# Performance work log

Measured on AMD Instinct MI355X. Metric: run time of the kernel, lower is better.

## Reference

```python
import jax, jax.numpy as jnp
import numpy as np

B, N, C, NH = 4, 2304, 256, 8
HD = C // NH            # head dim = 32
HS = WS = 48            # H = W = sqrt(N)
RADIUS = 3.0
MLP_HID = 4 * C
SCALE = HD ** (-0.5)
NEG = -1e9              # stands in for -inf (identical softmax up to fp eps)
EPS = 1e-6


def spatial_mask():
    # get_spatial_mask: cdist of (y, x) grid coords, -inf where dist > radius
    yy, xx = jnp.meshgrid(jnp.arange(HS), jnp.arange(WS), indexing='ij')
    coords = jnp.stack([yy, xx], -1).reshape(-1, 2).astype(jnp.float32)  # [N, 2]
    d2 = jnp.sum((coords[:, None, :] - coords[None, :, :]) ** 2, -1)     # [N, N]
    return jnp.where(d2 > RADIUS * RADIUS, NEG, 0.0)


def layernorm(x, g, b):
    mu = jnp.mean(x, -1, keepdims=True)
    var = jnp.mean((x - mu) ** 2, -1, keepdims=True)
    return (x - mu) * jax.lax.rsqrt(var + EPS) * g + b


def setup_inputs() -> dict:
    key = jax.random.key(0)
    ks = jax.random.split(key, 16)
    s = 0.02
    return {
        'x':    jax.random.normal(ks[0], (B, N, C), jnp.float32),
        'x_kv': jax.random.normal(ks[1], (B, N, C), jnp.float32),
        'Wq': jax.random.normal(ks[2], (C, C), jnp.float32) * s,
        'bq': jnp.zeros((C,), jnp.float32),
        'Wk': jax.random.normal(ks[3], (C, C), jnp.float32) * s,
        'bk': jnp.zeros((C,), jnp.float32),
        'Wv': jax.random.normal(ks[4], (C, C), jnp.float32) * s,
        'bv': jnp.zeros((C,), jnp.float32),
        'Wp': jax.random.normal(ks[5], (C, C), jnp.float32) * s,
        'bp': jnp.zeros((C,), jnp.float32),
        'g1': jnp.ones((C,), jnp.float32),
        'b1': jnp.zeros((C,), jnp.float32),
        'g2': jnp.ones((C,), jnp.float32),
        'b2': jnp.zeros((C,), jnp.float32),
        'W1': jax.random.normal(ks[6], (C, MLP_HID), jnp.float32) * s,
        'bm1': jnp.zeros((MLP_HID,), jnp.float32),
        'W2': jax.random.normal(ks[7], (MLP_HID, C), jnp.float32) * s,
        'bm2': jnp.zeros((C,), jnp.float32),
    }


def reference(x, x_kv, Wq, bq, Wk, bk, Wv, bv, Wp, bp,
              g1, b1, g2, b2, W1, bm1, W2, bm2):
    mask = spatial_mask()                                  # [N, N]
    h = layernorm(x, g1, b1)
    hkv = layernorm(x_kv, g1, b1)
    q = (h @ Wq + bq).reshape(B, N, NH, HD)
    k = (hkv @ Wk + bk).reshape(B, N, NH, HD)
    v = (hkv @ Wv + bv).reshape(B, N, NH, HD)
    scores = jnp.einsum('bqhd,bkhd->bhqk', q, k) * SCALE + mask
    attn = jax.nn.softmax(scores, axis=-1)
    out = jnp.einsum('bhqk,bkhd->bqhd', attn, v).reshape(B, N, C)
    x = x + out @ Wp + bp
    m = layernorm(x, g2, b2)
    x = x + jax.nn.gelu(m @ W1 + bm1, approximate=False) @ W2 + bm2
    return x
```

## Files before the change

### kernel.cpp

```cpp
#include <hip/hip_runtime.h>
#include <hip/hip_fp16.h>
#include <math.h>

#define BB 4
#define NN 2304
#define CC 256
#define HS 48
#define HID 1024
#define BNROWS (BB * NN)
#define ATTN_SCALE 0.17677669529663687f

typedef _Float16 f16;
typedef __attribute__((ext_vector_type(2))) _Float16 h2;
typedef __attribute__((ext_vector_type(8))) _Float16 h8;
typedef __attribute__((ext_vector_type(4))) float f4;

#define GLLS16(g, l)                                                        \
    __builtin_amdgcn_global_load_lds(                                       \
        (const __attribute__((address_space(1))) unsigned int*)(g),         \
        (__attribute__((address_space(3))) unsigned int*)(l), 16, 0, 0)
#define WAIT_VM0()   asm volatile("s_waitcnt vmcnt(0)" ::: "memory")
#define WAIT_VM6()   asm volatile("s_waitcnt vmcnt(6)" ::: "memory")
#define WAIT_LGKM0() asm volatile("s_waitcnt lgkmcnt(0)" ::: "memory")

static __device__ __forceinline__ float wave_sum64(float v) {
    v += __shfl_xor(v, 32, 64);
    v += __shfl_xor(v, 16, 64);
    v += __shfl_xor(v, 8, 64);
    v += __shfl_xor(v, 4, 64);
    v += __shfl_xor(v, 2, 64);
    v += __shfl_xor(v, 1, 64);
    return v;
}

__global__ __launch_bounds__(256) void prep_ln1_kernel(
    const float* __restrict__ x, const float* __restrict__ xkv,
    const float* __restrict__ Wq, const float* __restrict__ Wk,
    const float* __restrict__ Wv, const float* __restrict__ Wp,
    const float* __restrict__ W1, const float* __restrict__ W2,
    const float* __restrict__ bq, const float* __restrict__ bk,
    const float* __restrict__ bv,
    const float* __restrict__ g, const float* __restrict__ be,
    f16* __restrict__ WqkvT, f16* __restrict__ WpT,
    f16* __restrict__ W1T, f16* __restrict__ W2T, float* __restrict__ bqkv,
    f16* __restrict__ hq, f16* __restrict__ hkv)
{
    __shared__ float tt[32][33];
    int bx = blockIdx.x;
    const int tid = threadIdx.x;
    if (bx < 768) {
        const float* src; f16* dst; int K, N;
        if (bx < 64)        { src = Wq; dst = WqkvT;           K = 256;  N = 256; }
        else if (bx < 128)  { src = Wk; dst = WqkvT + 65536;   K = 256;  N = 256;  bx -= 64; }
        else if (bx < 192)  { src = Wv; dst = WqkvT + 131072;  K = 256;  N = 256;  bx -= 128; }
        else if (bx < 256)  { src = Wp; dst = WpT;             K = 256;  N = 256;  bx -= 192; }
        else if (bx < 512)  { src = W1; dst = W1T;             K = 256;  N = 1024; bx -= 256; }
        else                { src = W2; dst = W2T;             K = 1024; N = 256;  bx -= 512; }
        const int tN = N >> 5;
        const int kt = bx / tN, nt = bx - kt * tN;
        const int rr = tid >> 5, cc = tid & 31;
#pragma unroll
        for (int j = 0; j < 4; ++j)
            tt[rr + 8 * j][cc] = src[(size_t)(kt * 32 + rr + 8 * j) * N + nt * 32 + cc];
        __syncthreads();
#pragma unroll
        for (int j = 0; j < 4; ++j)
            dst[(size_t)(nt * 32 + rr + 8 * j) * K + kt * 32 + cc] = (f16)tt[cc][rr + 8 * j];
        return;
    }
    if (bx == 768) {
        if (tid < 256) {
            bqkv[tid]       = bq[tid];
            bqkv[tid + 256] = bk[tid];
            bqkv[tid + 512] = bv[tid];
        }
        return;
    }
    const int r = (bx - 769) * 4 + (tid >> 6);
    const int lane = tid & 63;
    const float* src; f16* dst;
    if (r < BNROWS) { src = x + (size_t)r * CC;              dst = hq + (size_t)r * CC; }
    else { src = xkv + (size_t)(r - BNROWS) * CC; dst = hkv + (size_t)(r - BNROWS) * CC; }
    const float4 v = ((const float4*)src)[lane];
    const float mu = wave_sum64(v.x + v.y + v.z + v.w) * (1.0f / CC);
    const float d0 = v.x - mu, d1 = v.y - mu, d2 = v.z - mu, d3 = v.w - mu;
    const float var = wave_sum64(d0 * d0 + d1 * d1 + d2 * d2 + d3 * d3) * (1.0f / CC);
    const float rs = rsqrtf(var + 1e-6f);
    const float4 g4 = ((const float4*)g)[lane];
    const float4 b4 = ((const float4*)be)[lane];
    h2 o01 = (h2){(f16)(d0 * rs * g4.x + b4.x), (f16)(d1 * rs * g4.y + b4.y)};
    h2 o23 = (h2){(f16)(d2 * rs * g4.z + b4.z), (f16)(d3 * rs * g4.w + b4.w)};
    ((h2*)dst)[lane * 2] = o01;
    ((h2*)dst)[lane * 2 + 1] = o23;
}

__global__ __launch_bounds__(256) void ln2_kernel(
    const f16* __restrict__ x1, const float* __restrict__ g,
    const float* __restrict__ be, f16* __restrict__ m2)
{
    const int r = blockIdx.x * 4 + (threadIdx.x >> 6);
    const int lane = threadIdx.x & 63;
    const f16* src = x1 + (size_t)r * CC;
    const h2 a01 = ((const h2*)src)[lane * 2];
    const h2 a23 = ((const h2*)src)[lane * 2 + 1];
    const float v0 = (float)a01[0], v1 = (float)a01[1];
    const float v2 = (float)a23[0], v3 = (float)a23[1];
    const float mu = wave_sum64(v0 + v1 + v2 + v3) * (1.0f / CC);
    const float d0 = v0 - mu, d1 = v1 - mu, d2 = v2 - mu, d3 = v3 - mu;
    const float var = wave_sum64(d0 * d0 + d1 * d1 + d2 * d2 + d3 * d3) * (1.0f / CC);
    const float rs = rsqrtf(var + 1e-6f);
    const float4 g4 = ((const float4*)g)[lane];
    const float4 b4 = ((const float4*)be)[lane];
    f16* dst = m2 + (size_t)r * CC;
    h2 o01 = (h2){(f16)(d0 * rs * g4.x + b4.x), (f16)(d1 * rs * g4.y + b4.y)};
    h2 o23 = (h2){(f16)(d2 * rs * g4.z + b4.z), (f16)(d3 * rs * g4.w + b4.w)};
    ((h2*)dst)[lane * 2] = o01;
    ((h2*)dst)[lane * 2 + 1] = o23;
}

template <bool GELU, int RESID, bool OUTF32, bool QKV>
__global__ __launch_bounds__(256, 4) void gemm_wave(
    const f16* __restrict__ Aq, const f16* __restrict__ Akv,
    const f16* __restrict__ Bt, const float* __restrict__ bias,
    const void* __restrict__ resid, void* __restrict__ out1,
    void* __restrict__ outkv, int N, int K)
{
    __shared__ f16 lds[4 * 6144];
    const int tid = threadIdx.x;
    const int wid = tid >> 6, lane = tid & 63;
    const int ln15 = lane & 15, quad = lane >> 4;
    const int jr = lane >> 2, js = lane & 3;
    f16* slot = lds + wid * 6144;
    const int n0 = blockIdx.x * 64;
    const int m0 = (blockIdx.y * 4 + wid) * 32;
    const f16* Ap = QKV ? (n0 < 256 ? Aq : Akv) : Aq;

    size_t ga[2], gb[4];
#pragma unroll
    for (int i = 0; i < 2; ++i) {
        const int r = i * 16 + jr;
        const int q = (js - (r >> 1)) & 3;
        ga[i] = (size_t)(m0 + r) * K + q * 8;
    }
#pragma unroll
    for (int i = 0; i < 4; ++i) {
        const int r = i * 16 + jr;
        const int q = (js - (r >> 1)) & 3;
        gb[i] = (size_t)(n0 + r) * K + q * 8;
    }
    int aoff[2], boff[4];
#pragma unroll
    for (int mt = 0; mt < 2; ++mt) {
        const int r = mt * 16 + ln15;
        aoff[mt] = (r * 4 + ((quad + (r >> 1)) & 3)) * 16;
    }
#pragma unroll
    for (int nt = 0; nt < 4; ++nt) {
        const int r = nt * 16 + ln15;
        boff[nt] = (r * 4 + ((quad + (r >> 1)) & 3)) * 16;
    }

    f4 acc[2][4];
#pragma unroll
    for (int i = 0; i < 2; ++i)
#pragma unroll
        for (int j = 0; j < 4; ++j) acc[i][j] = (f4){0.f, 0.f, 0.f, 0.f};

    {
        f16* Al = slot;
        f16* Bl = slot + 1024;
#pragma unroll
        for (int i = 0; i < 2; ++i) GLLS16(Ap + ga[i], Al + i * 512);
#pragma unroll
        for (int i = 0; i < 4; ++i) GLLS16(Bt + gb[i], Bl + i * 512);
    }

    int cur = 0;
    for (int k0 = 0; k0 < K; k0 += 32) {
        const bool more = (k0 + 32 < K);
        f16* Ac = slot + cur * 3072;
        f16* Bc = Ac + 1024;
        if (more) {
            f16* An = slot + (cur ^ 1) * 3072;
            f16* Bn = An + 1024;
            WAIT_LGKM0();
#pragma unroll
            for (int i = 0; i < 2; ++i) GLLS16(Ap + ga[i] + k0 + 32, An + i * 512);
#pragma unroll
            for (int i = 0; i < 4; ++i) GLLS16(Bt + gb[i] + k0 + 32, Bn + i * 512);
            WAIT_VM6();
        } else {
            WAIT_VM0();
        }
        h8 aF[2], bF[4];
#pragma unroll
        for (int nt = 0; nt < 4; ++nt)
            bF[nt] = *(const h8*)((const char*)Bc + boff[nt]);
#pragma unroll
        for (int mt = 0; mt < 2; ++mt)
            aF[mt] = *(const h8*)((const char*)Ac + aoff[mt]);
#pragma unroll
        for (int mt = 0; mt < 2; ++mt)
#pragma unroll
            for (int nt = 0; nt < 4; ++nt)
                acc[mt][nt] = __builtin_amdgcn_mfma_f32_16x16x32_f16(
                    aF[mt], bF[nt], acc[mt][nt], 0, 0, 0);
        cur ^= 1;
    }

#pragma unroll
    for (int nt = 0; nt < 4; ++nt) {
        const int gn = n0 + nt * 16 + ln15;
        const float bs = bias[gn];
#pragma unroll
        for (int mt = 0; mt < 2; ++mt) {
#pragma unroll
            for (int r = 0; r < 4; ++r) {
                const int gm = m0 + mt * 16 + quad * 4 + r;
                float v = acc[mt][nt][r] + bs;
                if (GELU) v = 0.5f * v * (1.0f + erff(v * 0.70710678118654752f));
                if (RESID == 1) v += ((const float*)resid)[(size_t)gm * N + gn];
                if (RESID == 2) v += (float)((const f16*)resid)[(size_t)gm * N + gn];
                if (QKV) {
                    if (gn < 256) ((f16*)out1)[(size_t)gm * 256 + gn] = (f16)v;
                    else ((f16*)outkv)[(size_t)gm * 512 + (gn - 256)] = (f16)v;
                } else if (OUTF32) {
                    ((float*)out1)[(size_t)gm * N + gn] = v;
                } else {
                    ((f16*)out1)[(size_t)gm * N + gn] = (f16)v;
                }
            }
        }
    }
}

__device__ __constant__ int ATT_DY[29] = {
    -3, -2, -2, -2, -2, -2, -1, -1, -1, -1, -1, 0, 0, 0, 0,
    0, 0, 0, 1, 1, 1, 1, 1, 2, 2, 2, 2, 2, 3};
__device__ __constant__ int ATT_DX[29] = {
    0, -2, -1, 0, 1, 2, -2, -1, 0, 1, 2, -3, -2, -1, 0,
    1, 2, 3, -2, -1, 0, 1, 2, -2, -1, 0, 1, 2, 0};

__global__ __launch_bounds__(128) void attn_tile_kernel(
    const f16* __restrict__ qf, const f16* __restrict__ kvf,
    f16* __restrict__ ao)
{
    __shared__ f16 ks[196][66];
    __shared__ f16 vs[196][66];
    const int tile = blockIdx.x, hp = blockIdx.y, b = blockIdx.z;
    const int ty0 = (tile / 6) * 8, tx0 = (tile - (tile / 6) * 6) * 8;
    const int tid = threadIdx.x;

    for (int idx = tid; idx < 196 * 16; idx += 128) {
        const int r = idx >> 4, seg = idx & 15;
        const int gy = ty0 - 3 + r / 14, gx = tx0 - 3 + (r - (r / 14) * 14);
        uint4 val = {0u, 0u, 0u, 0u};
        if ((unsigned)gy < HS && (unsigned)gx < HS) {
            const size_t rowb = ((size_t)b * NN + gy * HS + gx) * 512;
            const int ch = (seg < 8) ? (hp * 64 + seg * 8)
                                     : (256 + hp * 64 + (seg - 8) * 8);
            val = *(const uint4*)&kvf[rowb + ch];
        }
        f16* dstp = (seg < 8) ? &ks[r][(seg & 7) * 8] : &vs[r][(seg & 7) * 8];
        ((unsigned int*)dstp)[0] = val.x;
        ((unsigned int*)dstp)[1] = val.y;
        ((unsigned int*)dstp)[2] = val.z;
        ((unsigned int*)dstp)[3] = val.w;
    }
    __syncthreads();

    const int q = tid & 63, hh = tid >> 6;
    const int qy = q >> 3, qx = q & 7;
    const size_t qrow = (size_t)b * NN + (ty0 + qy) * HS + tx0 + qx;
    const f16* qp = qf + qrow * CC + hp * 64 + hh * 32;
    uint4 qa[4];
#pragma unroll
    for (int i = 0; i < 4; ++i) qa[i] = ((const uint4*)qp)[i];
    const h2* q2 = (const h2*)qa;

    float s[29];
#pragma unroll
    for (int n = 0; n < 29; ++n) {
        const int dy = ATT_DY[n], dx = ATT_DX[n];
        const int r = (qy + 3 + dy) * 14 + qx + 3 + dx;
        const bool valid = (unsigned)(ty0 + qy + dy) < HS &&
                           (unsigned)(tx0 + qx + dx) < HS;
        float a = 0.0f;
        const h2* kp = (const h2*)&ks[r][hh * 32];
#pragma unroll
        for (int i = 0; i < 16; ++i)
            a = __builtin_amdgcn_fdot2(q2[i], kp[i], a, false);
        s[n] = valid ? a * ATTN_SCALE : -1e30f;
    }
    float m = s[0];
#pragma unroll
    for (int n = 1; n < 29; ++n) m = fmaxf(m, s[n]);
    float l = 0.0f;
#pragma unroll
    for (int n = 0; n < 29; ++n) { s[n] = __expf(s[n] - m); l += s[n]; }
    h2 a2[16];
#pragma unroll
    for (int i = 0; i < 16; ++i) a2[i] = (h2){(f16)0.f, (f16)0.f};
#pragma unroll
    for (int n = 0; n < 29; ++n) {
        const int dy = ATT_DY[n], dx = ATT_DX[n];
        const int r = (qy + 3 + dy) * 14 + qx + 3 + dx;
        const f16 pn = (f16)s[n];
        const h2 ph = (h2){pn, pn};
        const h2* vp = (const h2*)&vs[r][hh * 32];
#pragma unroll
        for (int i = 0; i < 16; ++i) a2[i] += ph * vp[i];
    }
    const float inv = 1.0f / l;
    uint4 ov[4];
    f16* oh = (f16*)ov;
#pragma unroll
    for (int i = 0; i < 16; ++i) {
        oh[2 * i]     = (f16)((float)a2[i][0] * inv);
        oh[2 * i + 1] = (f16)((float)a2[i][1] * inv);
    }
    uint4* dst = (uint4*)(ao + qrow * CC + hp * 64 + hh * 32);
#pragma unroll
    for (int i = 0; i < 4; ++i) dst[i] = ov[i];
}

extern "C" void kernel_launch(void* const* d_in, const int* in_sizes, int n_in,
                              void* d_out, int out_size, void* d_ws, size_t ws_size,
                              hipStream_t stream) {
    const float* x    = (const float*)d_in[0];
    const float* x_kv = (const float*)d_in[1];
    const float* Wq   = (const float*)d_in[2];
    const float* bq   = (const float*)d_in[3];
    const float* Wk   = (const float*)d_in[4];
    const float* bk   = (const float*)d_in[5];
    const float* Wv   = (const float*)d_in[6];
    const float* bv   = (const float*)d_in[7];
    const float* Wp   = (const float*)d_in[8];
    const float* bp   = (const float*)d_in[9];
    const float* g1   = (const float*)d_in[10];
    const float* b1   = (const float*)d_in[11];
    const float* g2   = (const float*)d_in[12];
    const float* b2   = (const float*)d_in[13];
    const float* W1   = (const float*)d_in[14];
    const float* bm1  = (const float*)d_in[15];
    const float* W2   = (const float*)d_in[16];
    const float* bm2  = (const float*)d_in[17];
    float* outp = (float*)d_out;

    f16* wsh = (f16*)d_ws;
    f16* WqkvT = wsh;
    f16* WpT   = wsh + 196608;
    f16* W1T   = wsh + 262144;
    f16* W2T   = wsh + 524288;
    float* bqkv = (float*)(wsh + 786432);
    f16* hq    = wsh + 787968;
    f16* hkv   = wsh + 3147264;
    f16* qf    = wsh + 5506560;
    f16* kvf   = wsh + 7865856;
    f16* ao    = hq;
    f16* x1    = hkv;
    f16* m2    = qf;
    f16* hidF  = kvf;
    const bool fused = ws_size >= (size_t)17303040 * sizeof(f16);

    prep_ln1_kernel<<<5377, 256, 0, stream>>>(
        x, x_kv, Wq, Wk, Wv, Wp, W1, W2, bq, bk, bv, g1, b1,
        WqkvT, WpT, W1T, W2T, bqkv, hq, hkv);
    gemm_wave<false, 0, false, true><<<dim3(12, 72), 256, 0, stream>>>(
        hq, hkv, WqkvT, bqkv, nullptr, qf, kvf, 768, 256);
    attn_tile_kernel<<<dim3(36, 4, BB), 128, 0, stream>>>(qf, kvf, ao);
    gemm_wave<false, 1, false, false><<<dim3(4, 72), 256, 0, stream>>>(
        ao, nullptr, WpT, bp, x, x1, nullptr, 256, 256);
    ln2_kernel<<<BNROWS / 4, 256, 0, stream>>>(x1, g2, b2, m2);
    if (fused) {
        gemm_wave<true, 0, false, false><<<dim3(16, 72), 256, 0, stream>>>(
            m2, nullptr, W1T, bm1, nullptr, hidF, nullptr, 1024, 256);
        gemm_wave<false, 2, true, false><<<dim3(4, 72), 256, 0, stream>>>(
            hidF, nullptr, W2T, bm2, x1, outp, nullptr, 256, 1024);
    } else {
        for (int b = 0; b < BB; ++b) {
            const size_t off = (size_t)b * NN * CC;
            gemm_wave<true, 0, false, false><<<dim3(16, 18), 256, 0, stream>>>(
                m2 + off, nullptr, W1T, bm1, nullptr, hidF, nullptr, 1024, 256);
            gemm_wave<false, 2, true, false><<<dim3(4, 18), 256, 0, stream>>>(
                hidF, nullptr, W2T, bm2, x1 + off, outp + off, nullptr, 256, 1024);
        }
    }
    (void)in_sizes; (void)n_in; (void)out_size;
}
```

Measured before the change: 197.5 us.

## Fuse output projection GEMM with residual add and LayerNorm2 in one kernel

```diff
diff --git a/kernel.cpp b/kernel.cpp
--- a/kernel.cpp
+++ b/kernel.cpp
@@ -94,30 +94,6 @@
     ((h2*)dst)[lane * 2 + 1] = o23;
 }
 
-__global__ __launch_bounds__(256) void ln2_kernel(
-    const f16* __restrict__ x1, const float* __restrict__ g,
-    const float* __restrict__ be, f16* __restrict__ m2)
-{
-    const int r = blockIdx.x * 4 + (threadIdx.x >> 6);
-    const int lane = threadIdx.x & 63;
-    const f16* src = x1 + (size_t)r * CC;
-    const h2 a01 = ((const h2*)src)[lane * 2];
-    const h2 a23 = ((const h2*)src)[lane * 2 + 1];
-    const float v0 = (float)a01[0], v1 = (float)a01[1];
-    const float v2 = (float)a23[0], v3 = (float)a23[1];
-    const float mu = wave_sum64(v0 + v1 + v2 + v3) * (1.0f / CC);
-    const float d0 = v0 - mu, d1 = v1 - mu, d2 = v2 - mu, d3 = v3 - mu;
-    const float var = wave_sum64(d0 * d0 + d1 * d1 + d2 * d2 + d3 * d3) * (1.0f / CC);
-    const float rs = rsqrtf(var + 1e-6f);
-    const float4 g4 = ((const float4*)g)[lane];
-    const float4 b4 = ((const float4*)be)[lane];
-    f16* dst = m2 + (size_t)r * CC;
-    h2 o01 = (h2){(f16)(d0 * rs * g4.x + b4.x), (f16)(d1 * rs * g4.y + b4.y)};
-    h2 o23 = (h2){(f16)(d2 * rs * g4.z + b4.z), (f16)(d3 * rs * g4.w + b4.w)};
-    ((h2*)dst)[lane * 2] = o01;
-    ((h2*)dst)[lane * 2 + 1] = o23;
-}
-
 template <bool GELU, int RESID, bool OUTF32, bool QKV>
 __global__ __launch_bounds__(256, 4) void gemm_wave(
     const f16* __restrict__ Aq, const f16* __restrict__ Akv,
@@ -208,6 +184,11 @@
         cur ^= 1;
     }
 
+    f16* qdst = nullptr; int qstr = 0, qn0 = 0;
+    if (QKV) {
+        if (n0 < 256) { qdst = (f16*)out1;  qstr = 256; qn0 = n0; }
+        else          { qdst = (f16*)outkv; qstr = 512; qn0 = n0 - 256; }
+    }
 #pragma unroll
     for (int nt = 0; nt < 4; ++nt) {
         const int gn = n0 + nt * 16 + ln15;
@@ -222,13 +203,178 @@
                 if (RESID == 1) v += ((const float*)resid)[(size_t)gm * N + gn];
                 if (RESID == 2) v += (float)((const f16*)resid)[(size_t)gm * N + gn];
                 if (QKV) {
-                    if (gn < 256) ((f16*)out1)[(size_t)gm * 256 + gn] = (f16)v;
-                    else ((f16*)outkv)[(size_t)gm * 512 + (gn - 256)] = (f16)v;
+                    qdst[(size_t)gm * qstr + qn0 + nt * 16 + ln15] = (f16)v;
                 } else if (OUTF32) {
                     ((float*)out1)[(size_t)gm * N + gn] = v;
                 } else {
                     ((f16*)out1)[(size_t)gm * N + gn] = (f16)v;
                 }
+            }
+        }
+    }
+}
+
+__global__ __launch_bounds__(256, 3) void gemm_op_ln2(
+    const f16* __restrict__ Aa, const f16* __restrict__ Bt,
+    const float* __restrict__ bias, const float* __restrict__ xres,
+    const float* __restrict__ g, const float* __restrict__ be,
+    f16* __restrict__ x1, f16* __restrict__ m2)
+{
+    __shared__ f16 lds[4 * 6144];
+    __shared__ float sred[32][4][2];
+    const int tid = threadIdx.x;
+    const int wid = tid >> 6, lane = tid & 63;
+    const int ln15 = lane & 15, quad = lane >> 4;
+    const int jr = lane >> 2, js = lane & 3;
+    f16* slot = lds + wid * 6144;
+    const int m0 = blockIdx.x * 32;
+    const int n0 = wid * 64;
+    const int K = 256;
+
+    size_t ga[2], gb[4];
+#pragma unroll
+    for (int i = 0; i < 2; ++i) {
+        const int r = i * 16 + jr;
+        const int q = (js - (r >> 1)) & 3;
+        ga[i] = (size_t)(m0 + r) * K + q * 8;
+    }
+#pragma unroll
+    for (int i = 0; i < 4; ++i) {
+        const int r = i * 16 + jr;
+        const int q = (js - (r >> 1)) & 3;
+        gb[i] = (size_t)(n0 + r) * K + q * 8;
+    }
+    int aoff[2], boff[4];
+#pragma unroll
+    for (int mt = 0; mt < 2; ++mt) {
+        const int r = mt * 16 + ln15;
+        aoff[mt] = (r * 4 + ((quad + (r >> 1)) & 3)) * 16;
+    }
+#pragma unroll
+    for (int nt = 0; nt < 4; ++nt) {
+        const int r = nt * 16 + ln15;
+        boff[nt] = (r * 4 + ((quad + (r >> 1)) & 3)) * 16;
+    }
+
+    f4 acc[2][4];
+#pragma unroll
+    for (int i = 0; i < 2; ++i)
+#pragma unroll
+        for (int j = 0; j < 4; ++j) acc[i][j] = (f4){0.f, 0.f, 0.f, 0.f};
+
+    {
+        f16* Al = slot;
+        f16* Bl = slot + 1024;
+#pragma unroll
+        for (int i = 0; i < 2; ++i) GLLS16(Aa + ga[i], Al + i * 512);
+#pragma unroll
+        for (int i = 0; i < 4; ++i) GLLS16(Bt + gb[i], Bl + i * 512);
+    }
+    int cur = 0;
+    for (int k0 = 0; k0 < K; k0 += 32) {
+        const bool more = (k0 + 32 < K);
+        f16* Ac = slot + cur * 3072;
+        f16* Bc = Ac + 1024;
+        if (more) {
+            f16* An = slot + (cur ^ 1) * 3072;
+            f16* Bn = An + 1024;
+            WAIT_LGKM0();
+#pragma unroll
+            for (int i = 0; i < 2; ++i) GLLS16(Aa + ga[i] + k0 + 32, An + i * 512);
+#pragma unroll
+            for (int i = 0; i < 4; ++i) GLLS16(Bt + gb[i] + k0 + 32, Bn + i * 512);
+            WAIT_VM6();
+        } else {
+            WAIT_VM0();
+        }
+        h8 aF[2], bF[4];
+#pragma unroll
+        for (int nt = 0; nt < 4; ++nt)
+            bF[nt] = *(const h8*)((const char*)Bc + boff[nt]);
+#pragma unroll
+        for (int mt = 0; mt < 2; ++mt)
+            aF[mt] = *(const h8*)((const char*)Ac + aoff[mt]);
+#pragma unroll
+        for (int mt = 0; mt < 2; ++mt)
+#pragma unroll
+            for (int nt = 0; nt < 4; ++nt)
+                acc[mt][nt] = __builtin_amdgcn_mfma_f32_16x16x32_f16(
+                    aF[mt], bF[nt], acc[mt][nt], 0, 0, 0);
+        cur ^= 1;
+    }
+
+    float bsv[4], g2v[4], b2v[4];
+#pragma unroll
+    for (int nt = 0; nt < 4; ++nt) {
+        const int gn = n0 + nt * 16 + ln15;
+        bsv[nt] = bias[gn];
+        g2v[nt] = g[gn];
+        b2v[nt] = be[gn];
+    }
+    float s1[2][4], s2[2][4];
+#pragma unroll
+    for (int mt = 0; mt < 2; ++mt)
+#pragma unroll
+        for (int r = 0; r < 4; ++r) { s1[mt][r] = 0.f; s2[mt][r] = 0.f; }
+#pragma unroll
+    for (int mt = 0; mt < 2; ++mt) {
+#pragma unroll
+        for (int r = 0; r < 4; ++r) {
+            const int gm = m0 + mt * 16 + quad * 4 + r;
+#pragma unroll
+            for (int nt = 0; nt < 4; ++nt) {
+                const int gn = n0 + nt * 16 + ln15;
+                float v = acc[mt][nt][r] + bsv[nt]
+                        + xres[(size_t)gm * CC + gn];
+                acc[mt][nt][r] = v;
+                x1[(size_t)gm * CC + gn] = (f16)v;
+                s1[mt][r] += v;
+                s2[mt][r] += v * v;
+            }
+        }
+    }
+#pragma unroll
+    for (int off = 1; off < 16; off <<= 1) {
+#pragma unroll
+        for (int mt = 0; mt < 2; ++mt)
+#pragma unroll
+            for (int r = 0; r < 4; ++r) {
+                s1[mt][r] += __shfl_xor(s1[mt][r], off, 64);
+                s2[mt][r] += __shfl_xor(s2[mt][r], off, 64);
+            }
+    }
+    if (ln15 == 0) {
+#pragma unroll
+        for (int mt = 0; mt < 2; ++mt)
+#pragma unroll
+            for (int r = 0; r < 4; ++r) {
+                const int rr = mt * 16 + quad * 4 + r;
+                sred[rr][wid][0] = s1[mt][r];
+                sred[rr][wid][1] = s2[mt][r];
+            }
+    }
+    __syncthreads();
+#pragma unroll
+    for (int mt = 0; mt < 2; ++mt) {
+#pragma unroll
+        for (int r = 0; r < 4; ++r) {
+            const int rr = mt * 16 + quad * 4 + r;
+            const int gm = m0 + rr;
+            float a = 0.f, b = 0.f;
+#pragma unroll
+            for (int w = 0; w < 4; ++w) {
+                a += sred[rr][w][0];
+                b += sred[rr][w][1];
+            }
+            const float mu = a * (1.0f / CC);
+            const float var = fmaxf(b * (1.0f / CC) - mu * mu, 0.0f);
+            const float rs = rsqrtf(var + 1e-6f);
+#pragma unroll
+            for (int nt = 0; nt < 4; ++nt) {
+                const int gn = n0 + nt * 16 + ln15;
+                const float v = acc[mt][nt][r];
+                m2[(size_t)gm * CC + gn] =
+                    (f16)((v - mu) * rs * g2v[nt] + b2v[nt]);
             }
         }
     }
@@ -369,9 +515,7 @@
     gemm_wave<false, 0, false, true><<<dim3(12, 72), 256, 0, stream>>>(
         hq, hkv, WqkvT, bqkv, nullptr, qf, kvf, 768, 256);
     attn_tile_kernel<<<dim3(36, 4, BB), 128, 0, stream>>>(qf, kvf, ao);
-    gemm_wave<false, 1, false, false><<<dim3(4, 72), 256, 0, stream>>>(
-        ao, nullptr, WpT, bp, x, x1, nullptr, 256, 256);
-    ln2_kernel<<<BNROWS / 4, 256, 0, stream>>>(x1, g2, b2, m2);
+    gemm_op_ln2<<<288, 256, 0, stream>>>(ao, WpT, bp, x, g2, b2, x1, m2);
     if (fused) {
         gemm_wave<true, 0, false, false><<<dim3(16, 72), 256, 0, stream>>>(
             m2, nullptr, W1T, bm1, nullptr, hidF, nullptr, 1024, 256);
```

Measured after the change: 195.3 us. No clear change (-1.1%).
